# Performance work log

Hardware: AMD Instinct MI355X
Metric: run time of the kernel (lower is better)

Reference implementation:

```python
import jax, jax.numpy as jnp
import numpy as np

N = 50000        # nodes
E = 400000       # edges
F_IN = 128       # node feature dim
NEG_SLOPE = 0.2  # PyG GATConv default


def setup_inputs() -> dict:
    key = jax.random.key(0)
    ks = jax.random.split(key, 24)
    p = lambda k, shape: (jax.random.normal(k, shape, dtype=jnp.float32) * 0.1)
    return {
        "x": jax.random.normal(ks[0], (N, F_IN), dtype=jnp.float32),
        "edge_index": jax.random.randint(ks[1], (2, E), 0, N, dtype=jnp.int32),
        "edge_attr": jax.random.normal(ks[2], (E, 1), dtype=jnp.float32),
        "year": jax.random.normal(ks[3], (E, 1), dtype=jnp.float32),
        "quarter": jax.random.normal(ks[4], (E, 1), dtype=jnp.float32),
        "W1": p(ks[5], (4 * 128, F_IN)), "a1s": p(ks[6], (4, 128)), "a1d": p(ks[7], (4, 128)), "b1": jnp.zeros((512,), jnp.float32),
        "W2": p(ks[8], (4 * 32, 512)), "a2s": p(ks[9], (4, 32)), "a2d": p(ks[10], (4, 32)), "b2": jnp.zeros((128,), jnp.float32),
        "W3": p(ks[11], (1 * 8, 128)), "a3s": p(ks[12], (1, 8)), "a3d": p(ks[13], (1, 8)), "b3": jnp.zeros((8,), jnp.float32),
        # fc1: 8*2 + 1 + 2 = 19 -> 16 ; fc2: 16 -> 1
        "fc1_w": p(ks[14], (16, 19)), "fc1_b": jnp.zeros((16,), jnp.float32),
        "fc2_w": p(ks[15], (1, 16)), "fc2_b": jnp.zeros((1,), jnp.float32),
    }


def gat_conv(x, src, dst, W, a_s, a_d, b):
    """PyG GATConv (concat=True, self-loops already in src/dst, no dropout)."""
    H, C = a_s.shape
    n = x.shape[0]
    h = (x @ W.T).reshape(n, H, C)                      # [N,H,C]
    s = jnp.einsum("nhc,hc->nh", h, a_s)                # alpha_src per node
    d = jnp.einsum("nhc,hc->nh", h, a_d)                # alpha_dst per node
    e = jax.nn.leaky_relu(s[src] + d[dst], NEG_SLOPE)   # [E',H]
    m = jax.ops.segment_max(e, dst, num_segments=n)     # segment softmax over dst
    ex = jnp.exp(e - m[dst])
    den = jax.ops.segment_sum(ex, dst, num_segments=n)
    alpha = ex / den[dst]                               # [E',H]
    out = jax.ops.segment_sum(alpha[:, :, None] * h[src], dst, num_segments=n)
    return out.reshape(n, H * C) + b


def reference(x, edge_index, edge_attr, year, quarter,
              W1, a1s, a1d, b1, W2, a2s, a2d, b2, W3, a3s, a3d, b3,
              fc1_w, fc1_b, fc2_w, fc2_b):
    n = x.shape[0]
    loops = jnp.arange(n, dtype=edge_index.dtype)       # add_self_loops=True
    src = jnp.concatenate([edge_index[0], loops])
    dst = jnp.concatenate([edge_index[1], loops])
    h = jax.nn.elu(gat_conv(x, src, dst, W1, a1s, a1d, b1))
    h = jax.nn.elu(gat_conv(h, src, dst, W2, a2s, a2d, b2))
    h = jax.nn.elu(gat_conv(h, src, dst, W3, a3s, a3d, b3))
    z = jnp.concatenate([h[edge_index[0]], h[edge_index[1]], edge_attr, year, quarter], axis=1)
    z = jax.nn.relu(z @ fc1_w.T + fc1_b)
    return (z @ fc2_w.T + fc2_b).squeeze(-1)            # [E]
```

## Files before the change

### kernel.cpp

```cpp
#include <hip/hip_runtime.h>
#include <hip/hip_bf16.h>

#define NN 50000
#define EE 400000
#define EP 450000

typedef __attribute__((ext_vector_type(8))) short short8;
typedef __attribute__((ext_vector_type(4))) float f32x4;

__device__ __forceinline__ float us2f(unsigned short u) {
    unsigned int x = ((unsigned int)u) << 16;
    union { unsigned int i; float f; } c; c.i = x; return c.f;
}
__device__ __forceinline__ unsigned short f2bfu(float f) {
    union { float f; unsigned int u; } c; c.f = f;
    unsigned int r = c.u + 0x7FFFu + ((c.u >> 16) & 1u);
    return (unsigned short)(r >> 16);
}
__device__ __forceinline__ float lrelu_exp(float x) {
    x = x > 0.f ? x : 0.2f * x;
    return __expf(x);
}


#define DEGB 1758
#define CVTB 512
__global__ void prep_kernel(const int* __restrict__ ei, int* __restrict__ deg,
                            const float* __restrict__ W1, const float* __restrict__ W2,
                            __hip_bfloat16* __restrict__ pw1, __hip_bfloat16* __restrict__ pw2,
                            const float* __restrict__ a1s, const float* __restrict__ a1d,
                            float* __restrict__ usd) {
    int b = blockIdx.x;
    if (b < DEGB) {
        int e = b * 256 + threadIdx.x;
        if (e >= EP) return;
        int dst = (e < EE) ? ei[EE + e] : e - EE;
        atomicAdd(&deg[dst], 1);
    } else if (b < DEGB + CVTB) {
        int i = (b - DEGB) * 256 + threadIdx.x;
        if (i < 65536) {
            int n = i >> 7, k = i & 127;
            int idx = ((n >> 4) * 4 + (k >> 5)) * 512 + ((k & 31) >> 3) * 128 + (n & 15) * 8 + (k & 7);
            pw1[idx] = __float2bfloat16(W1[i]);
        } else {
            int j = i - 65536;
            int n = j >> 9, k = j & 511;
            int idx = ((n >> 4) * 16 + (k >> 5)) * 512 + ((k & 31) >> 3) * 128 + (n & 15) * 8 + (k & 7);
            pw2[idx] = __float2bfloat16(W2[j]);
        }
    } else {
        int t = (b - DEGB - CVTB) * 256 + threadIdx.x;
        if (t >= 1024) return;
        int row = t >> 7, k = t & 127;
        int hh = row & 3;
        const float* av = (row < 4) ? (a1s + hh * 128) : (a1d + hh * 128);
        const float* wp = W1 + (size_t)(hh * 128) * 128 + k;
        float acc = 0.f;
        for (int c = 0; c < 128; c++) acc += av[c] * wp[(size_t)c * 128];
        usd[t] = acc;
    }
}

__global__ void cvtx_sd(const float* __restrict__ x, const float* __restrict__ usd,
                        __hip_bfloat16* __restrict__ xb,
                        float* __restrict__ s, float* __restrict__ d, int M) {
    __shared__ float us_s[1024];
    for (int i = threadIdx.x; i < 1024; i += 256) us_s[i] = usd[i];
    __syncthreads();
    int wave = threadIdx.x >> 6, lane = threadIdx.x & 63;
    int m0 = blockIdx.x * 64 + wave * 16;
    int r = lane & 15, quad = lane >> 4;
    int am = m0 + r; if (am >= M) am = M - 1;
    const float* xp = x + (size_t)am * 128 + quad * 8;
    float xv[32];
#pragma unroll
    for (int kk = 0; kk < 4; kk++) {
        float4 a = *(const float4*)(xp + kk * 32);
        float4 bq = *(const float4*)(xp + kk * 32 + 4);
        xv[kk*8+0]=a.x;  xv[kk*8+1]=a.y;  xv[kk*8+2]=a.z;  xv[kk*8+3]=a.w;
        xv[kk*8+4]=bq.x; xv[kk*8+5]=bq.y; xv[kk*8+6]=bq.z; xv[kk*8+7]=bq.w;
        short8 o;
        o[0]=(short)f2bfu(a.x);  o[1]=(short)f2bfu(a.y);
        o[2]=(short)f2bfu(a.z);  o[3]=(short)f2bfu(a.w);
        o[4]=(short)f2bfu(bq.x); o[5]=(short)f2bfu(bq.y);
        o[6]=(short)f2bfu(bq.z); o[7]=(short)f2bfu(bq.w);
        *(short8*)(xb + (size_t)am * 128 + quad * 8 + kk * 32) = o;
    }
    float acc[8];
#pragma unroll
    for (int o = 0; o < 8; o++) {
        const float* up = us_s + o * 128 + quad * 8;
        float a = 0.f;
#pragma unroll
        for (int kk = 0; kk < 4; kk++)
#pragma unroll
            for (int j = 0; j < 8; j++) a += xv[kk*8+j] * up[kk*32+j];
        acc[o] = a;
    }
#pragma unroll
    for (int o = 0; o < 8; o++) {
        acc[o] += __shfl_xor(acc[o], 16, 64);
        acc[o] += __shfl_xor(acc[o], 32, 64);
    }
    int m = m0 + r;
    if (quad == 0 && m < M) {
#pragma unroll
        for (int hh = 0; hh < 4; hh++) { s[m*4+hh] = acc[hh]; d[m*4+hh] = acc[4+hh]; }
    }
}

#define SCB 49
__global__ void scan1_kernel(const int* __restrict__ deg, int* __restrict__ bsum) {
    __shared__ int red[256];
    int b = blockIdx.x, t = threadIdx.x;
    int base = b * 1024 + t * 4;
    int s = 0;
    if (base + 3 < NN) { int4 v = *(const int4*)(deg + base); s = v.x + v.y + v.z + v.w; }
    else { for (int i = base; i < NN; i++) s += deg[i]; }
    red[t] = s;
    __syncthreads();
    for (int off = 128; off > 0; off >>= 1) {
        if (t < off) red[t] += red[t + off];
        __syncthreads();
    }
    if (t == 0) bsum[b] = red[0];
}

__global__ void scan2_kernel(const int* __restrict__ deg, const int* __restrict__ bsum,
                             int* __restrict__ offsets) {
    __shared__ int lsum[256];
    int b = blockIdx.x, t = threadIdx.x;
    int boff = 0;
    for (int i = 0; i < b; i++) boff += bsum[i];
    int base = b * 1024 + t * 4;
    int4 v = {0, 0, 0, 0};
    if (base + 3 < NN) v = *(const int4*)(deg + base);
    else {
        if (base < NN)     v.x = deg[base];
        if (base + 1 < NN) v.y = deg[base + 1];
        if (base + 2 < NN) v.z = deg[base + 2];
        if (base + 3 < NN) v.w = deg[base + 3];
    }
    int s = v.x + v.y + v.z + v.w;
    lsum[t] = s;
    __syncthreads();
    for (int off = 1; off < 256; off <<= 1) {
        int val = (t >= off) ? lsum[t - off] : 0;
        __syncthreads();
        lsum[t] += val;
        __syncthreads();
    }
    int ex = boff + (t ? lsum[t - 1] : 0);
    if (base < NN)     offsets[base]     = ex;
    if (base + 1 < NN) offsets[base + 1] = ex + v.x;
    if (base + 2 < NN) offsets[base + 2] = ex + v.x + v.y;
    if (base + 3 < NN) offsets[base + 3] = ex + v.x + v.y + v.z;
    if (b == SCB - 1 && t == 255) offsets[NN] = boff + lsum[255];
}

__global__ void fill_kernel(const int* __restrict__ ei, const int* __restrict__ offsets,
                            int* __restrict__ cursor,
                            const float* __restrict__ s1, const float* __restrict__ d1,
                            int* __restrict__ elist, int* __restrict__ dstlist,
                            float* __restrict__ welist) {
    int e = blockIdx.x * blockDim.x + threadIdx.x;
    if (e >= EP) return;
    int src, dst;
    if (e < EE) { src = ei[e]; dst = ei[EE + e]; } else { src = dst = e - EE; }
    int pos = atomicAdd(&cursor[dst], 1);
    int j = offsets[dst] + pos;
    elist[j] = src;
    dstlist[j] = dst;
    float4 sv = *(const float4*)(s1 + (size_t)src * 4);
    float4 dv = *(const float4*)(d1 + (size_t)dst * 4);
    float4 w;
    w.x = lrelu_exp(sv.x + dv.x);
    w.y = lrelu_exp(sv.y + dv.y);
    w.z = lrelu_exp(sv.z + dv.z);
    w.w = lrelu_exp(sv.w + dv.w);
    *(float4*)(welist + (size_t)j * 4) = w;
}

__global__ void edge_w4(const int* __restrict__ elist, const int* __restrict__ dstlist,
                        const float* __restrict__ s, const float* __restrict__ d,
                        float* __restrict__ wout) {
    int j = blockIdx.x * blockDim.x + threadIdx.x;
    if (j >= EP) return;
    int src = elist[j], dst = dstlist[j];
    float4 sv = *(const float4*)(s + (size_t)src * 4);
    float4 dv = *(const float4*)(d + (size_t)dst * 4);
    float4 w;
    w.x = lrelu_exp(sv.x + dv.x);
    w.y = lrelu_exp(sv.y + dv.y);
    w.z = lrelu_exp(sv.z + dv.z);
    w.w = lrelu_exp(sv.w + dv.w);
    *(float4*)(wout + (size_t)j * 4) = w;
}

__global__ void edge_w1(const int* __restrict__ elist, const int* __restrict__ dstlist,
                        const float* __restrict__ s, const float* __restrict__ d,
                        float* __restrict__ wout) {
    int j = blockIdx.x * blockDim.x + threadIdx.x;
    if (j >= EP) return;
    wout[j] = lrelu_exp(s[elist[j]] + d[dstlist[j]]);
}

__global__ void gather_agg(const int* __restrict__ elist, const int* __restrict__ offsets,
                           const float* __restrict__ wl,
                           const __hip_bfloat16* __restrict__ xb,
                           __hip_bfloat16* __restrict__ pagg) {
    int wid = blockIdx.x * 4 + (threadIdx.x >> 6);
    if (wid >= NN) return;
    int lane = threadIdx.x & 63;
    int node = wid;
    int j0 = __builtin_amdgcn_readfirstlane(offsets[node]);
    int j1 = __builtin_amdgcn_readfirstlane(offsets[node + 1]);
    float den0 = 0.f, den1 = 0.f, den2 = 0.f, den3 = 0.f;
    float a00=0.f,a01=0.f,a10=0.f,a11=0.f,a20=0.f,a21=0.f,a30=0.f,a31=0.f;
    const unsigned short* xp = (const unsigned short*)xb + lane * 2;
    int j = j0;
    for (; j + 4 <= j1; j += 4) {
        int sA = elist[j], sB = elist[j+1], sC = elist[j+2], sD = elist[j+3];
        float4 wA = *(const float4*)(wl + (size_t)j * 4);
        float4 wB = *(const float4*)(wl + (size_t)(j+1) * 4);
        float4 wC = *(const float4*)(wl + (size_t)(j+2) * 4);
        float4 wD = *(const float4*)(wl + (size_t)(j+3) * 4);
        unsigned int xA = *(const unsigned int*)(xp + (size_t)sA * 128);
        unsigned int xB = *(const unsigned int*)(xp + (size_t)sB * 128);
        unsigned int xC = *(const unsigned int*)(xp + (size_t)sC * 128);
        unsigned int xD = *(const unsigned int*)(xp + (size_t)sD * 128);
        float xA0 = us2f((unsigned short)xA), xA1 = us2f((unsigned short)(xA >> 16));
        float xB0 = us2f((unsigned short)xB), xB1 = us2f((unsigned short)(xB >> 16));
        float xC0 = us2f((unsigned short)xC), xC1 = us2f((unsigned short)(xC >> 16));
        float xD0 = us2f((unsigned short)xD), xD1 = us2f((unsigned short)(xD >> 16));
        den0 += (wA.x + wB.x) + (wC.x + wD.x);
        den1 += (wA.y + wB.y) + (wC.y + wD.y);
        den2 += (wA.z + wB.z) + (wC.z + wD.z);
        den3 += (wA.w + wB.w) + (wC.w + wD.w);
        a00 += wA.x*xA0 + wB.x*xB0 + wC.x*xC0 + wD.x*xD0;
        a01 += wA.x*xA1 + wB.x*xB1 + wC.x*xC1 + wD.x*xD1;
        a10 += wA.y*xA0 + wB.y*xB0 + wC.y*xC0 + wD.y*xD0;
        a11 += wA.y*xA1 + wB.y*xB1 + wC.y*xC1 + wD.y*xD1;
        a20 += wA.z*xA0 + wB.z*xB0 + wC.z*xC0 + wD.z*xD0;
        a21 += wA.z*xA1 + wB.z*xB1 + wC.z*xC1 + wD.z*xD1;
        a30 += wA.w*xA0 + wB.w*xB0 + wC.w*xC0 + wD.w*xD0;
        a31 += wA.w*xA1 + wB.w*xB1 + wC.w*xC1 + wD.w*xD1;
    }
    for (; j < j1; j++) {
        int sE = elist[j];
        float4 w = *(const float4*)(wl + (size_t)j * 4);
        unsigned int xv = *(const unsigned int*)(xp + (size_t)sE * 128);
        float x0 = us2f((unsigned short)xv), x1 = us2f((unsigned short)(xv >> 16));
        den0 += w.x; den1 += w.y; den2 += w.z; den3 += w.w;
        a00 += w.x*x0; a01 += w.x*x1; a10 += w.y*x0; a11 += w.y*x1;
        a20 += w.z*x0; a21 += w.z*x1; a30 += w.w*x0; a31 += w.w*x1;
    }
    int c0 = lane * 2;
    int fq = c0 >> 5;
    size_t tb = (size_t)(node >> 4) * 16 * 512 + (size_t)((c0 & 31) >> 3) * 128
              + (size_t)(node & 15) * 8 + (c0 & 7);
    unsigned short* pb = (unsigned short*)pagg + tb;
    float i0 = 1.f/den0, i1 = 1.f/den1, i2 = 1.f/den2, i3 = 1.f/den3;
    *(unsigned int*)(pb + (size_t)(0*4 + fq) * 512) =
        (unsigned int)f2bfu(a00*i0) | ((unsigned int)f2bfu(a01*i0) << 16);
    *(unsigned int*)(pb + (size_t)(1*4 + fq) * 512) =
        (unsigned int)f2bfu(a10*i1) | ((unsigned int)f2bfu(a11*i1) << 16);
    *(unsigned int*)(pb + (size_t)(2*4 + fq) * 512) =
        (unsigned int)f2bfu(a20*i2) | ((unsigned int)f2bfu(a21*i2) << 16);
    *(unsigned int*)(pb + (size_t)(3*4 + fq) * 512) =
        (unsigned int)f2bfu(a30*i3) | ((unsigned int)f2bfu(a31*i3) << 16);
}

__global__ void gemm_bdiag(const __hip_bfloat16* __restrict__ pA,
                           const __hip_bfloat16* __restrict__ pW1,
                           const float* __restrict__ b,
                           __hip_bfloat16* __restrict__ pact, int M) {
    int hh = threadIdx.x >> 6, lane = threadIdx.x & 63;
    int m0 = blockIdx.x * 16;
    int r = lane & 15, quad = lane >> 4;
    short8 afrag[4];
    const __hip_bfloat16* ap = pA + ((size_t)(m0 >> 4) * 16 + hh * 4) * 512 + lane * 8;
#pragma unroll
    for (int kk = 0; kk < 4; kk++) afrag[kk] = *(const short8*)(ap + kk * 512);
#pragma unroll
    for (int nb = 0; nb < 128; nb += 16) {
        const __hip_bfloat16* bp = pW1 + ((size_t)(hh * 8 + (nb >> 4)) * 4) * 512 + lane * 8;
        f32x4 acc = {0.f, 0.f, 0.f, 0.f};
#pragma unroll
        for (int kk = 0; kk < 4; kk++) {
            short8 bfr = *(const short8*)(bp + kk * 512);
            acc = __builtin_amdgcn_mfma_f32_16x16x32_bf16(afrag[kk], bfr, acc, 0, 0, 0);
        }
        int n0 = hh * 128 + nb;
        float bias = b[n0 + r];
        int kk2 = (n0 + r) >> 5;
        int sub = ((nb & 16) + r) >> 3;
        __hip_bfloat16* op = pact + ((size_t)(m0 >> 4) * 16 + kk2) * 512
                           + sub * 128 + (r & 7);
#pragma unroll
        for (int i = 0; i < 4; i++) {
            float v = acc[i] + bias;
            v = v > 0.f ? v : (__expf(v) - 1.0f);
            op[(quad * 4 + i) * 8] = __float2bfloat16(v);
        }
    }
}

__global__ void gemm_l2(const __hip_bfloat16* __restrict__ pA,
                        const __hip_bfloat16* __restrict__ pW2,
                        const float* __restrict__ as_, const float* __restrict__ ad_,
                        __hip_bfloat16* __restrict__ Cb,
                        float* __restrict__ s, float* __restrict__ d, int M) {
    int hh = threadIdx.x >> 6, lane = threadIdx.x & 63;
    int m0 = blockIdx.x * 16;
    int r = lane & 15, quad = lane >> 4;
    const __hip_bfloat16* ap  = pA + (size_t)(m0 >> 4) * 16 * 512 + lane * 8;
    const __hip_bfloat16* bp0 = pW2 + (size_t)(hh * 2) * 16 * 512 + lane * 8;
    const __hip_bfloat16* bp1 = bp0 + 16 * 512;
    f32x4 acc0 = {0.f, 0.f, 0.f, 0.f}, acc1 = {0.f, 0.f, 0.f, 0.f};
#pragma unroll
    for (int kk = 0; kk < 16; kk++) {
        short8 af = *(const short8*)(ap + kk * 512);
        short8 b0 = *(const short8*)(bp0 + kk * 512);
        short8 b1 = *(const short8*)(bp1 + kk * 512);
        acc0 = __builtin_amdgcn_mfma_f32_16x16x32_bf16(af, b0, acc0, 0, 0, 0);
        acc1 = __builtin_amdgcn_mfma_f32_16x16x32_bf16(af, b1, acc1, 0, 0, 0);
    }
    int n0 = hh * 32;
    float as0 = as_[n0 + r],      ad0 = ad_[n0 + r];
    float as1 = as_[n0 + 16 + r], ad1 = ad_[n0 + 16 + r];
    float sacc[4], dacc[4];
#pragma unroll
    for (int i = 0; i < 4; i++) {
        int m = m0 + quad * 4 + i;
        Cb[(size_t)m * 128 + n0 + r]      = __float2bfloat16(acc0[i]);
        Cb[(size_t)m * 128 + n0 + 16 + r] = __float2bfloat16(acc1[i]);
        sacc[i] = acc0[i] * as0 + acc1[i] * as1;
        dacc[i] = acc0[i] * ad0 + acc1[i] * ad1;
    }
#pragma unroll
    for (int mask = 1; mask <= 8; mask <<= 1) {
#pragma unroll
        for (int i = 0; i < 4; i++) {
            sacc[i] += __shfl_xor(sacc[i], mask, 64);
            dacc[i] += __shfl_xor(dacc[i], mask, 64);
        }
    }
    if (r == 0) {
#pragma unroll
        for (int i = 0; i < 4; i++) {
            int m = m0 + quad * 4 + i;
            s[m * 4 + hh] = sacc[i]; d[m * 4 + hh] = dacc[i];
        }
    }
}

__global__ void gather_l2(const int* __restrict__ elist, const int* __restrict__ offsets,
                          const float* __restrict__ wl,
                          const __hip_bfloat16* __restrict__ h,
                          const float* __restrict__ b,
                          __hip_bfloat16* __restrict__ act) {
    int gid = blockIdx.x * blockDim.x + threadIdx.x;
    if (gid >= NN * 64) return;
    int node = gid >> 6;
    int lane = gid & 63;
    int c0 = lane * 2;
    int hh = lane >> 4;
    int j0 = __builtin_amdgcn_readfirstlane(offsets[node]);
    int j1 = __builtin_amdgcn_readfirstlane(offsets[node + 1]);
    float den = 0.f, acc0 = 0.f, acc1 = 0.f;
    const unsigned short* hp = (const unsigned short*)h + c0;
    int j = j0;
    for (; j + 4 <= j1; j += 4) {
        int sA = elist[j], sB = elist[j+1], sC = elist[j+2], sD = elist[j+3];
        float wA = wl[(size_t)j*4 + hh],     wB = wl[(size_t)(j+1)*4 + hh];
        float wC = wl[(size_t)(j+2)*4 + hh], wD = wl[(size_t)(j+3)*4 + hh];
        unsigned int vA = *(const unsigned int*)(hp + (size_t)sA * 128);
        unsigned int vB = *(const unsigned int*)(hp + (size_t)sB * 128);
        unsigned int vC = *(const unsigned int*)(hp + (size_t)sC * 128);
        unsigned int vD = *(const unsigned int*)(hp + (size_t)sD * 128);
        den += (wA + wB) + (wC + wD);
        acc0 += wA * us2f((unsigned short)vA) + wB * us2f((unsigned short)vB)
              + wC * us2f((unsigned short)vC) + wD * us2f((unsigned short)vD);
        acc1 += wA * us2f((unsigned short)(vA >> 16)) + wB * us2f((unsigned short)(vB >> 16))
              + wC * us2f((unsigned short)(vC >> 16)) + wD * us2f((unsigned short)(vD >> 16));
    }
    for (; j < j1; j++) {
        int sE = elist[j];
        float w = wl[(size_t)j*4 + hh];
        unsigned int v = *(const unsigned int*)(hp + (size_t)sE * 128);
        den += w;
        acc0 += w * us2f((unsigned short)v);
        acc1 += w * us2f((unsigned short)(v >> 16));
    }
    float inv = 1.0f / den;
    float v0 = acc0 * inv + b[c0];
    float v1 = acc1 * inv + b[c0 + 1];
    v0 = v0 > 0.f ? v0 : (__expf(v0) - 1.0f);
    v1 = v1 > 0.f ? v1 : (__expf(v1) - 1.0f);
    *(unsigned int*)((unsigned short*)act + (size_t)node * 128 + c0) =
        (unsigned int)f2bfu(v0) | ((unsigned int)f2bfu(v1) << 16);
}

__global__ void gather_l3(const int* __restrict__ elist, const int* __restrict__ offsets,
                          const float* __restrict__ wl,
                          const __hip_bfloat16* __restrict__ h,
                          const float* __restrict__ b,
                          __hip_bfloat16* __restrict__ act) {
    int gid = blockIdx.x * blockDim.x + threadIdx.x;
    if (gid >= NN * 8) return;
    int node = gid >> 3, t = gid & 7;
    int j0 = offsets[node], j1 = offsets[node + 1];
    float den = 0.f, acc = 0.f;
    const unsigned short* hp = (const unsigned short*)h + t;
    int j = j0;
    for (; j + 4 <= j1; j += 4) {
        int sA = elist[j], sB = elist[j+1], sC = elist[j+2], sD = elist[j+3];
        float wA = wl[j], wB = wl[j+1], wC = wl[j+2], wD = wl[j+3];
        float xA = us2f(hp[(size_t)sA * 8]);
        float xB = us2f(hp[(size_t)sB * 8]);
        float xC = us2f(hp[(size_t)sC * 8]);
        float xD = us2f(hp[(size_t)sD * 8]);
        den += (wA + wB) + (wC + wD);
        acc += wA * xA + wB * xB + wC * xC + wD * xD;
    }
    for (; j < j1; j++) {
        int sE = elist[j];
        float w = wl[j];
        den += w;
        acc += w * us2f(hp[(size_t)sE * 8]);
    }
    float v = acc / den + b[t];
    v = v > 0.f ? v : (__expf(v) - 1.0f);
    act[(size_t)node * 8 + t] = __float2bfloat16(v);
}

__global__ void gemm8_kernel(const __hip_bfloat16* __restrict__ A,
                             const float* __restrict__ W,
                             const float* __restrict__ a3s, const float* __restrict__ a3d,
                             __hip_bfloat16* __restrict__ Cb,
                             float* __restrict__ s, float* __restrict__ d) {
    int gid = blockIdx.x * blockDim.x + threadIdx.x;
    if (gid >= NN * 8) return;
    int n = gid >> 3, t = gid & 7;
    const unsigned short* ap = (const unsigned short*)A + (size_t)n * 128 + t * 16;
    short8 v0 = *(const short8*)ap;
    short8 v1 = *(const short8*)(ap + 8);
    float xf[16];
#pragma unroll
    for (int j = 0; j < 8; j++) { xf[j] = us2f((unsigned short)v0[j]); xf[8+j] = us2f((unsigned short)v1[j]); }
    float acc[8];
#pragma unroll
    for (int c = 0; c < 8; c++) {
        const float* wp = W + c * 128 + t * 16;
        float a = 0.f;
#pragma unroll
        for (int j = 0; j < 16; j++) a += xf[j] * wp[j];
        acc[c] = a;
    }
#pragma unroll
    for (int mask = 1; mask <= 4; mask <<= 1)
#pragma unroll
        for (int c = 0; c < 8; c++) acc[c] += __shfl_xor(acc[c], mask, 64);
    Cb[n * 8 + t] = __float2bfloat16(acc[t]);
    if (t == 0) {
        float sv = 0.f, dvv = 0.f;
#pragma unroll
        for (int c = 0; c < 8; c++) { sv += acc[c] * a3s[c]; dvv += acc[c] * a3d[c]; }
        s[n] = sv; d[n] = dvv;
    }
}

__global__ void mlp_kernel(const int* __restrict__ ei,
                           const __hip_bfloat16* __restrict__ act3,
                           const float* __restrict__ ea,
                           const float* __restrict__ yr,
                           const float* __restrict__ qt,
                           const float* __restrict__ fc1w,
                           const float* __restrict__ fc1b,
                           const float* __restrict__ fc2w,
                           const float* __restrict__ fc2b,
                           float* __restrict__ outp) {
    __shared__ float w1[16 * 19], b1s[16], w2[16];
    for (int i = threadIdx.x; i < 16 * 19; i += blockDim.x) w1[i] = fc1w[i];
    if (threadIdx.x < 16) {
        b1s[threadIdx.x] = fc1b[threadIdx.x];
        w2[threadIdx.x] = fc2w[threadIdx.x];
    }
    __syncthreads();
    int e = blockIdx.x * blockDim.x + threadIdx.x;
    if (e >= EE) return;
    int src = ei[e], dst = ei[EE + e];
    short8 hs = *(const short8*)(act3 + (size_t)src * 8);
    short8 hd = *(const short8*)(act3 + (size_t)dst * 8);
    float z[19];
#pragma unroll
    for (int i = 0; i < 8; i++) z[i] = us2f((unsigned short)hs[i]);
#pragma unroll
    for (int i = 0; i < 8; i++) z[8 + i] = us2f((unsigned short)hd[i]);
    z[16] = ea[e]; z[17] = yr[e]; z[18] = qt[e];
    float acc2 = fc2b[0];
#pragma unroll
    for (int j = 0; j < 16; j++) {
        float a = b1s[j];
#pragma unroll
        for (int i = 0; i < 19; i++) a += z[i] * w1[j * 19 + i];
        a = a > 0.f ? a : 0.f;
        acc2 += a * w2[j];
    }
    outp[e] = acc2;
}

extern "C" void kernel_launch(void* const* d_in, const int* in_sizes, int n_in,
                              void* d_out, int out_size, void* d_ws, size_t ws_size,
                              hipStream_t stream) {
    const float* x    = (const float*)d_in[0];
    const int*   ei   = (const int*)d_in[1];
    const float* ea   = (const float*)d_in[2];
    const float* yr   = (const float*)d_in[3];
    const float* qt   = (const float*)d_in[4];
    const float* W1   = (const float*)d_in[5];
    const float* a1s  = (const float*)d_in[6];
    const float* a1d  = (const float*)d_in[7];
    const float* b1   = (const float*)d_in[8];
    const float* W2   = (const float*)d_in[9];
    const float* a2s  = (const float*)d_in[10];
    const float* a2d  = (const float*)d_in[11];
    const float* b2   = (const float*)d_in[12];
    const float* W3   = (const float*)d_in[13];
    const float* a3s  = (const float*)d_in[14];
    const float* a3d  = (const float*)d_in[15];
    const float* b3   = (const float*)d_in[16];
    const float* fc1w = (const float*)d_in[17];
    const float* fc1b = (const float*)d_in[18];
    const float* fc2w = (const float*)d_in[19];
    const float* fc2b = (const float*)d_in[20];
    float* outp = (float*)d_out;

    char* ws = (char*)d_ws;
    __hip_bfloat16* h_buf   = (__hip_bfloat16*)(ws);
    __hip_bfloat16* act_buf = (__hip_bfloat16*)(ws + 51200000);
    float* s_buf   = (float*)(ws + 102400000);
    float* d_buf   = (float*)(ws + 103200000);
    int*   deg     = (int*)  (ws + 104000000);
    int*   cursor  = (int*)  (ws + 104200000);
    int*   offsets = (int*)  (ws + 104400000);
    int*   elist   = (int*)  (ws + 104600016);
    __hip_bfloat16* pw1 = (__hip_bfloat16*)(ws + 106400016);
    __hip_bfloat16* pw2 = (__hip_bfloat16*)(ws + 106531088);
    float* usd  = (float*)(ws + 106662160);
    int*   bsum = (int*)  (ws + 106666256);
    float* welist = (float*)(ws + 106666512);
    int*   dstlist = (int*)(ws + 113866512);
    __hip_bfloat16* xb = act_buf;

    hipMemsetAsync(deg, 0, 2 * NN * sizeof(int), stream);
    prep_kernel<<<DEGB + CVTB + 4, 256, 0, stream>>>(ei, deg, W1, W2, pw1, pw2, a1s, a1d, usd);
    scan1_kernel<<<SCB, 256, 0, stream>>>(deg, bsum);
    scan2_kernel<<<SCB, 256, 0, stream>>>(deg, bsum, offsets);
    cvtx_sd<<<(NN + 63) / 64, 256, 0, stream>>>(x, usd, xb, s_buf, d_buf, NN);
    fill_kernel<<<(EP + 255) / 256, 256, 0, stream>>>(ei, offsets, cursor, s_buf, d_buf,
                                                      elist, dstlist, welist);

    gather_agg<<<(NN + 3) / 4, 256, 0, stream>>>(elist, offsets, welist, xb, h_buf);
    gemm_bdiag<<<(NN + 15) / 16, 256, 0, stream>>>(h_buf, pw1, b1, act_buf, NN);

    gemm_l2<<<(NN + 15) / 16, 256, 0, stream>>>(
        act_buf, pw2, a2s, a2d, h_buf, s_buf, d_buf, NN);
    edge_w4<<<(EP + 255) / 256, 256, 0, stream>>>(elist, dstlist, s_buf, d_buf, welist);
    gather_l2<<<(NN * 64 + 255) / 256, 256, 0, stream>>>(
        elist, offsets, welist, h_buf, b2, act_buf);

    gemm8_kernel<<<(NN * 8 + 255) / 256, 256, 0, stream>>>(
        act_buf, W3, a3s, a3d, h_buf, s_buf, d_buf);
    edge_w1<<<(EP + 255) / 256, 256, 0, stream>>>(elist, dstlist, s_buf, d_buf, welist);
    gather_l3<<<(NN * 8 + 255) / 256, 256, 0, stream>>>(
        elist, offsets, welist, h_buf, b3, act_buf);

    mlp_kernel<<<(EE + 255) / 256, 256, 0, stream>>>(ei, act_buf, ea, yr, qt,
                                                     fc1w, fc1b, fc2w, fc2b, outp);
}
```

Before: 332.5 us.

## Fuse layer-1 gather with block-diagonal GEMM and layer-2 gather with layer-3 projection

Merges the layer-1 neighbour aggregation and the per-head MFMA GEMM into one 1024-thread kernel. The aggregated bf16 tile is staged in swizzled shared memory, so it no longer round-trips through global memory. Separately, the layer-2 gather now applies the 8-wide W3 projection and the attention score dot products itself through a full wave shuffle reduction, which removes the gemm8 kernel launch and its reread of the activations. The costs are lower occupancy from large blocks, a block-wide barrier, and more shuffle work per node. The activation and hidden buffers swap roles to match.

```diff
diff --git a/kernel.cpp b/kernel.cpp
--- a/kernel.cpp
+++ b/kernel.cpp
@@ -16,6 +16,9 @@
     union { float f; unsigned int u; } c; c.f = f;
     unsigned int r = c.u + 0x7FFFu + ((c.u >> 16) & 1u);
     return (unsigned short)(r >> 16);
+}
+__device__ __forceinline__ unsigned int pack2bf(float lo, float hi) {
+    return (unsigned int)f2bfu(lo) | ((unsigned int)f2bfu(hi) << 16);
 }
 __device__ __forceinline__ float lrelu_exp(float x) {
     x = x > 0.f ? x : 0.2f * x;
@@ -205,14 +208,18 @@
     wout[j] = lrelu_exp(s[elist[j]] + d[dstlist[j]]);
 }
 
-__global__ void gather_agg(const int* __restrict__ elist, const int* __restrict__ offsets,
-                           const float* __restrict__ wl,
-                           const __hip_bfloat16* __restrict__ xb,
-                           __hip_bfloat16* __restrict__ pagg) {
-    int wid = blockIdx.x * 4 + (threadIdx.x >> 6);
-    if (wid >= NN) return;
-    int lane = threadIdx.x & 63;
-    int node = wid;
+__global__ __launch_bounds__(1024) void l1_fused(
+        const int* __restrict__ elist, const int* __restrict__ offsets,
+        const float* __restrict__ wl,
+        const __hip_bfloat16* __restrict__ xb,
+        const __hip_bfloat16* __restrict__ pW1,
+        const float* __restrict__ b,
+        __hip_bfloat16* __restrict__ pact) {
+    __shared__ unsigned short frag[16 * 520];
+    int w = threadIdx.x >> 6, lane = threadIdx.x & 63;
+    int m0 = blockIdx.x * 16;
+    int node = m0 + w;
+
     int j0 = __builtin_amdgcn_readfirstlane(offsets[node]);
     int j1 = __builtin_amdgcn_readfirstlane(offsets[node + 1]);
     float den0 = 0.f, den1 = 0.f, den2 = 0.f, den3 = 0.f;
@@ -248,42 +255,40 @@
     }
     for (; j < j1; j++) {
         int sE = elist[j];
-        float4 w = *(const float4*)(wl + (size_t)j * 4);
+        float4 ww = *(const float4*)(wl + (size_t)j * 4);
         unsigned int xv = *(const unsigned int*)(xp + (size_t)sE * 128);
         float x0 = us2f((unsigned short)xv), x1 = us2f((unsigned short)(xv >> 16));
-        den0 += w.x; den1 += w.y; den2 += w.z; den3 += w.w;
-        a00 += w.x*x0; a01 += w.x*x1; a10 += w.y*x0; a11 += w.y*x1;
-        a20 += w.z*x0; a21 += w.z*x1; a30 += w.w*x0; a31 += w.w*x1;
-    }
-    int c0 = lane * 2;
-    int fq = c0 >> 5;
-    size_t tb = (size_t)(node >> 4) * 16 * 512 + (size_t)((c0 & 31) >> 3) * 128
-              + (size_t)(node & 15) * 8 + (c0 & 7);
-    unsigned short* pb = (unsigned short*)pagg + tb;
-    float i0 = 1.f/den0, i1 = 1.f/den1, i2 = 1.f/den2, i3 = 1.f/den3;
-    *(unsigned int*)(pb + (size_t)(0*4 + fq) * 512) =
-        (unsigned int)f2bfu(a00*i0) | ((unsigned int)f2bfu(a01*i0) << 16);
-    *(unsigned int*)(pb + (size_t)(1*4 + fq) * 512) =
-        (unsigned int)f2bfu(a10*i1) | ((unsigned int)f2bfu(a11*i1) << 16);
-    *(unsigned int*)(pb + (size_t)(2*4 + fq) * 512) =
-        (unsigned int)f2bfu(a20*i2) | ((unsigned int)f2bfu(a21*i2) << 16);
-    *(unsigned int*)(pb + (size_t)(3*4 + fq) * 512) =
-        (unsigned int)f2bfu(a30*i3) | ((unsigned int)f2bfu(a31*i3) << 16);
-}
-
-__global__ void gemm_bdiag(const __hip_bfloat16* __restrict__ pA,
-                           const __hip_bfloat16* __restrict__ pW1,
-                           const float* __restrict__ b,
-                           __hip_bfloat16* __restrict__ pact, int M) {
-    int hh = threadIdx.x >> 6, lane = threadIdx.x & 63;
-    int m0 = blockIdx.x * 16;
+        den0 += ww.x; den1 += ww.y; den2 += ww.z; den3 += ww.w;
+        a00 += ww.x*x0; a01 += ww.x*x1; a10 += ww.y*x0; a11 += ww.y*x1;
+        a20 += ww.z*x0; a21 += ww.z*x1; a30 += ww.w*x0; a31 += ww.w*x1;
+    }
+    {
+        int c0 = lane * 2;
+        int fq = c0 >> 5;
+        int sub = (c0 & 31) >> 3;
+        int rowp = w ^ (sub << 2);
+        float i0 = 1.f/den0, i1 = 1.f/den1, i2 = 1.f/den2, i3 = 1.f/den3;
+        unsigned int* f32p = (unsigned int*)frag;
+        int base = (fq * 520 + sub * 128 + rowp * 8 + (c0 & 7)) >> 1;
+        f32p[base]             = pack2bf(a00*i0, a01*i0);
+        f32p[base + 4 * 260]   = pack2bf(a10*i1, a11*i1);
+        f32p[base + 8 * 260]   = pack2bf(a20*i2, a21*i2);
+        f32p[base + 12 * 260]  = pack2bf(a30*i3, a31*i3);
+    }
+    __syncthreads();
+
+    int hh = w >> 2, g = w & 3;
     int r = lane & 15, quad = lane >> 4;
+    int lsub = lane >> 4, lrow = lane & 15;
+    int prow = lrow ^ (lsub << 2);
+    const unsigned short* fb = frag + lsub * 128 + prow * 8;
     short8 afrag[4];
-    const __hip_bfloat16* ap = pA + ((size_t)(m0 >> 4) * 16 + hh * 4) * 512 + lane * 8;
-#pragma unroll
-    for (int kk = 0; kk < 4; kk++) afrag[kk] = *(const short8*)(ap + kk * 512);
-#pragma unroll
-    for (int nb = 0; nb < 128; nb += 16) {
+#pragma unroll
+    for (int kk = 0; kk < 4; kk++)
+        afrag[kk] = *(const short8*)(fb + (hh * 4 + kk) * 520);
+#pragma unroll
+    for (int t = 0; t < 2; t++) {
+        int nb = g * 32 + t * 16;
         const __hip_bfloat16* bp = pW1 + ((size_t)(hh * 8 + (nb >> 4)) * 4) * 512 + lane * 8;
         f32x4 acc = {0.f, 0.f, 0.f, 0.f};
 #pragma unroll
@@ -294,9 +299,9 @@
         int n0 = hh * 128 + nb;
         float bias = b[n0 + r];
         int kk2 = (n0 + r) >> 5;
-        int sub = ((nb & 16) + r) >> 3;
-        __hip_bfloat16* op = pact + ((size_t)(m0 >> 4) * 16 + kk2) * 512
-                           + sub * 128 + (r & 7);
+        int sub2 = ((nb & 16) + r) >> 3;
+        __hip_bfloat16* op = pact + ((size_t)blockIdx.x * 16 + kk2) * 512
+                           + sub2 * 128 + (r & 7);
 #pragma unroll
         for (int i = 0; i < 4; i++) {
             float v = acc[i] + bias;
@@ -355,11 +360,14 @@
     }
 }
 
-__global__ void gather_l2(const int* __restrict__ elist, const int* __restrict__ offsets,
-                          const float* __restrict__ wl,
-                          const __hip_bfloat16* __restrict__ h,
-                          const float* __restrict__ b,
-                          __hip_bfloat16* __restrict__ act) {
+__global__ void gather_l2_g8(const int* __restrict__ elist, const int* __restrict__ offsets,
+                             const float* __restrict__ wl,
+                             const __hip_bfloat16* __restrict__ h,
+                             const float* __restrict__ b,
+                             const float* __restrict__ W3,
+                             const float* __restrict__ a3s, const float* __restrict__ a3d,
+                             __hip_bfloat16* __restrict__ h3,
+                             float* __restrict__ s, float* __restrict__ d) {
     int gid = blockIdx.x * blockDim.x + threadIdx.x;
     if (gid >= NN * 64) return;
     int node = gid >> 6;
@@ -387,19 +395,35 @@
     }
     for (; j < j1; j++) {
         int sE = elist[j];
-        float w = wl[(size_t)j*4 + hh];
+        float ww = wl[(size_t)j*4 + hh];
         unsigned int v = *(const unsigned int*)(hp + (size_t)sE * 128);
-        den += w;
-        acc0 += w * us2f((unsigned short)v);
-        acc1 += w * us2f((unsigned short)(v >> 16));
+        den += ww;
+        acc0 += ww * us2f((unsigned short)v);
+        acc1 += ww * us2f((unsigned short)(v >> 16));
     }
     float inv = 1.0f / den;
     float v0 = acc0 * inv + b[c0];
     float v1 = acc1 * inv + b[c0 + 1];
     v0 = v0 > 0.f ? v0 : (__expf(v0) - 1.0f);
     v1 = v1 > 0.f ? v1 : (__expf(v1) - 1.0f);
-    *(unsigned int*)((unsigned short*)act + (size_t)node * 128 + c0) =
-        (unsigned int)f2bfu(v0) | ((unsigned int)f2bfu(v1) << 16);
+    float part[8];
+#pragma unroll
+    for (int c = 0; c < 8; c++) {
+        float2 wv = *(const float2*)(W3 + c * 128 + c0);
+        part[c] = v0 * wv.x + v1 * wv.y;
+    }
+#pragma unroll
+    for (int mask = 1; mask < 64; mask <<= 1) {
+#pragma unroll
+        for (int c = 0; c < 8; c++) part[c] += __shfl_xor(part[c], mask, 64);
+    }
+    if (lane < 8) h3[(size_t)node * 8 + lane] = __float2bfloat16(part[lane]);
+    if (lane == 0) {
+        float sv = 0.f, dv = 0.f;
+#pragma unroll
+        for (int c = 0; c < 8; c++) { sv += part[c] * a3s[c]; dv += part[c] * a3d[c]; }
+        s[node] = sv; d[node] = dv;
+    }
 }
 
 __global__ void gather_l3(const int* __restrict__ elist, const int* __restrict__ offsets,
@@ -433,42 +457,6 @@
     float v = acc / den + b[t];
     v = v > 0.f ? v : (__expf(v) - 1.0f);
     act[(size_t)node * 8 + t] = __float2bfloat16(v);
-}
-
-__global__ void gemm8_kernel(const __hip_bfloat16* __restrict__ A,
-                             const float* __restrict__ W,
-                             const float* __restrict__ a3s, const float* __restrict__ a3d,
-                             __hip_bfloat16* __restrict__ Cb,
-                             float* __restrict__ s, float* __restrict__ d) {
-    int gid = blockIdx.x * blockDim.x + threadIdx.x;
-    if (gid >= NN * 8) return;
-    int n = gid >> 3, t = gid & 7;
-    const unsigned short* ap = (const unsigned short*)A + (size_t)n * 128 + t * 16;
-    short8 v0 = *(const short8*)ap;
-    short8 v1 = *(const short8*)(ap + 8);
-    float xf[16];
-#pragma unroll
-    for (int j = 0; j < 8; j++) { xf[j] = us2f((unsigned short)v0[j]); xf[8+j] = us2f((unsigned short)v1[j]); }
-    float acc[8];
-#pragma unroll
-    for (int c = 0; c < 8; c++) {
-        const float* wp = W + c * 128 + t * 16;
-        float a = 0.f;
-#pragma unroll
-        for (int j = 0; j < 16; j++) a += xf[j] * wp[j];
-        acc[c] = a;
-    }
-#pragma unroll
-    for (int mask = 1; mask <= 4; mask <<= 1)
-#pragma unroll
-        for (int c = 0; c < 8; c++) acc[c] += __shfl_xor(acc[c], mask, 64);
-    Cb[n * 8 + t] = __float2bfloat16(acc[t]);
-    if (t == 0) {
-        float sv = 0.f, dvv = 0.f;
-#pragma unroll
-        for (int c = 0; c < 8; c++) { sv += acc[c] * a3s[c]; dvv += acc[c] * a3d[c]; }
-        s[n] = sv; d[n] = dvv;
-    }
 }
 
 __global__ void mlp_kernel(const int* __restrict__ ei,
@@ -562,17 +550,15 @@
     fill_kernel<<<(EP + 255) / 256, 256, 0, stream>>>(ei, offsets, cursor, s_buf, d_buf,
                                                       elist, dstlist, welist);
 
-    gather_agg<<<(NN + 3) / 4, 256, 0, stream>>>(elist, offsets, welist, xb, h_buf);
-    gemm_bdiag<<<(NN + 15) / 16, 256, 0, stream>>>(h_buf, pw1, b1, act_buf, NN);
+    l1_fused<<<NN / 16, 1024, 0, stream>>>(elist, offsets, welist, xb, pw1, b1, h_buf);
 
     gemm_l2<<<(NN + 15) / 16, 256, 0, stream>>>(
-        act_buf, pw2, a2s, a2d, h_buf, s_buf, d_buf, NN);
+        h_buf, pw2, a2s, a2d, act_buf, s_buf, d_buf, NN);
     edge_w4<<<(EP + 255) / 256, 256, 0, stream>>>(elist, dstlist, s_buf, d_buf, welist);
-    gather_l2<<<(NN * 64 + 255) / 256, 256, 0, stream>>>(
-        elist, offsets, welist, h_buf, b2, act_buf);
-
-    gemm8_kernel<<<(NN * 8 + 255) / 256, 256, 0, stream>>>(
-        act_buf, W3, a3s, a3d, h_buf, s_buf, d_buf);
+
+    gather_l2_g8<<<(NN * 64 + 255) / 256, 256, 0, stream>>>(
+        elist, offsets, welist, act_buf, b2, W3, a3s, a3d, h_buf, s_buf, d_buf);
+
     edge_w1<<<(EP + 255) / 256, 256, 0, stream>>>(elist, dstlist, s_buf, d_buf, welist);
     gather_l3<<<(NN * 8 + 255) / 256, 256, 0, stream>>>(
         elist, offsets, welist, h_buf, b3, act_buf);
```

Measured after the change: 308.4 us. 7.3% less time.
